# Kernel tuning notes

Measured on AMD Instinct MI355X. Metric: run time of the kernel, lower is better.

Reference implementation:

```python
import jax, jax.numpy as jnp
import numpy as np

KD_T = 4.0
PATCH_NUM = 64
MASK_NUM = 8
BATCH = 256
DIM = 2048
P = PATCH_NUM - MASK_NUM  # 56


def setup_inputs() -> dict:
    key = jax.random.key(0)
    k1, k2, k3 = jax.random.split(key, 3)
    ebg = jax.random.normal(k1, (BATCH, DIM), dtype=jnp.float32)
    ebp = jax.random.normal(k2, (P * BATCH, DIM), dtype=jnp.float32)
    labels = jax.random.randint(k3, (BATCH,), 0, 10, dtype=jnp.int64)
    return {"ebg": ebg, "ebp": ebp, "labels": labels}


def _kl(y_s, y_t, T):
    # Faithful to KLDiv with dim=0 on vectors: softmax over the feature axis,
    # F.kl_div(..., reduction='batchmean') on a length-D vector divides by D.
    D = y_s.shape[-1]
    log_p_s = jax.nn.log_softmax(y_s / T, axis=-1)
    log_p_t = jax.nn.log_softmax(y_t / T, axis=-1)
    p_t = jnp.exp(log_p_t)
    return jnp.sum(p_t * (log_p_t - log_p_s), axis=-1) * (T * T / D)


def reference(ebg, ebp, labels):
    sg = jax.lax.stop_gradient
    ebp_r = ebp.reshape(P, BATCH, DIM)          # [P, B, D]
    ebp_bar = ebp_r.mean(axis=0)                # [B, D]

    # soft_dil_loss: sum over batch of symmetric KD with detached targets
    soft_dil = jnp.sum(_kl(ebg, sg(ebp_bar), KD_T)) + jnp.sum(_kl(ebp_bar, sg(ebg), KD_T))

    # soft_dcl_loss: per (batch, patch) pair on squared differences
    ebp_t = jnp.transpose(ebp_r, (1, 0, 2))     # [B, P, D]
    dg = (ebg[:, None, :] - ebp_t) ** 2         # [B, P, D]
    db = (ebp_bar[:, None, :] - ebp_t) ** 2     # [B, P, D]
    soft_dcl = (jnp.sum(_kl(dg, db, KD_T)) + jnp.sum(_kl(db, dg, KD_T))) / P

    return (soft_dil, soft_dcl)
```

## Files before the change

### kernel.cpp

```cpp
#include <hip/hip_runtime.h>
#include <math.h>

#define DIM    2048
#define BATCH  256
#define PN     56
#define CHUNK  128
#define NCHUNK 4
#define NQ     4
#define QCOLS  (CHUNK * NCHUNK)
#define NBLK   (BATCH * NQ)
constexpr float KD_T = 4.0f;

__device__ __forceinline__ float wave_sum(float v) {
#pragma unroll
    for (int o = 32; o > 0; o >>= 1) v += __shfl_xor(v, o, 64);
    return v;
}
__device__ __forceinline__ float half_sum(float v) {
#pragma unroll
    for (int o = 16; o > 0; o >>= 1) v += __shfl_xor(v, o, 64);
    return v;
}
__device__ __forceinline__ double wave_sum_d(double v) {
#pragma unroll
    for (int o = 32; o > 0; o >>= 1) v += __shfl_xor(v, o, 64);
    return v;
}

__global__ void __launch_bounds__(256) fused_kernel(const float* __restrict__ ebg,
                                                    const float* __restrict__ ebp,
                                                    float* __restrict__ pdcl,
                                                    float* __restrict__ pdil,
                                                    double* __restrict__ dcl_acc,
                                                    unsigned* __restrict__ ticket)
{
    __shared__ float  ebp_s[PN * CHUNK];
    __shared__ float4 redbar[4][32];
    __shared__ float  bar_s[CHUNK];
    __shared__ float  redl[4][4];

    const int t    = threadIdx.x;
    const int lane = t & 63;
    const int wv   = t >> 6;
    const int sub  = lane >> 5;
    const int c32  = lane & 31;
    const int bid  = blockIdx.x;
    const int b    = bid >> 2;
    const int q    = bid & (NQ - 1);
    const float invT = 1.0f / KD_T;

    if (bid == 0 && t == 0) { *dcl_acc = 0.0; *ticket = 0u; }

    const size_t rowoff = (size_t)b * DIM + (size_t)q * QCOLS;

    float acc[7][4];
#pragma unroll
    for (int j = 0; j < 7; ++j)
#pragma unroll
        for (int k = 0; k < 4; ++k) acc[j][k] = 0.f;

    float dss = 0.f, dts = 0.f, dt1 = 0.f, dt2 = 0.f;

    for (int c = 0; c < NCHUNK; ++c) {
        const size_t cb = rowoff + (size_t)c * CHUNK;

        const int prow0 = t >> 5;
        const int cc4   = (t & 31) * 4;
        float4 vals[7];
#pragma unroll
        for (int it = 0; it < 7; ++it) {
            const int p = it * 8 + prow0;
            vals[it] = *(const float4*)(ebp + (size_t)p * (BATCH * DIM) + cb + cc4);
        }
        float4 bp = {0.f, 0.f, 0.f, 0.f};
#pragma unroll
        for (int it = 0; it < 7; ++it) {
            const int p = it * 8 + prow0;
            *(float4*)(ebp_s + p * CHUNK + cc4) = vals[it];
            bp.x += vals[it].x; bp.y += vals[it].y;
            bp.z += vals[it].z; bp.w += vals[it].w;
        }
        bp.x += __shfl_xor(bp.x, 32, 64);
        bp.y += __shfl_xor(bp.y, 32, 64);
        bp.z += __shfl_xor(bp.z, 32, 64);
        bp.w += __shfl_xor(bp.w, 32, 64);
        if (lane < 32) redbar[wv][lane] = bp;
        __syncthreads();
        if (t < 32) {
            float4 s0 = redbar[0][t], s1 = redbar[1][t],
                   s2 = redbar[2][t], s3 = redbar[3][t];
            float4 s;
            s.x = (s0.x + s1.x + s2.x + s3.x) * (1.0f / PN);
            s.y = (s0.y + s1.y + s2.y + s3.y) * (1.0f / PN);
            s.z = (s0.z + s1.z + s2.z + s3.z) * (1.0f / PN);
            s.w = (s0.w + s1.w + s2.w + s3.w) * (1.0f / PN);
            *(float4*)(bar_s + t * 4) = s;
        }
        __syncthreads();

        if (t < CHUNK) {
            float g = ebg[cb + t];
            float m = bar_s[t];
            float s = g * invT, tv = m * invT;
            float es = __expf(s), et = __expf(tv);
            float dd = tv - s;
            dss += es; dts += et;
            dt1 = fmaf(es, dd, dt1);
            dt2 = fmaf(et, dd, dt2);
        }

        const float4 g4 = *(const float4*)(ebg + cb + c32 * 4);
        const float4 m4 = *(const float4*)(bar_s + c32 * 4);
        const float gs[4] = {g4.x, g4.y, g4.z, g4.w};
        const float ms[4] = {m4.x, m4.y, m4.z, m4.w};
#pragma unroll
        for (int j = 0; j < 7; ++j) {
            const int row = wv * 14 + 2 * j + sub;
            float4 e = *(const float4*)(ebp_s + row * CHUNK + c32 * 4);
            float es_[4] = {e.x, e.y, e.z, e.w};
#pragma unroll
            for (int k = 0; k < 4; ++k) {
                float dg = gs[k] - es_[k];
                float db = ms[k] - es_[k];
                float a  = dg * dg * invT;
                float cc = db * db * invT;
                float ea = __expf(a), ec = __expf(cc);
                float d  = cc - a;
                acc[j][0] += ea;
                acc[j][1] += ec;
                acc[j][2] = fmaf(ea, d, acc[j][2]);
                acc[j][3] = fmaf(ec, d, acc[j][3]);
            }
        }
        __syncthreads();
    }

#pragma unroll
    for (int j = 0; j < 7; ++j) {
        float a0 = half_sum(acc[j][0]);
        float a1 = half_sum(acc[j][1]);
        float a2 = half_sum(acc[j][2]);
        float a3 = half_sum(acc[j][3]);
        if (c32 == 0) {
            const int row = wv * 14 + 2 * j + sub;
            float* qp = pdcl + (((size_t)row * BATCH + b) * NQ + q) * 4;
            qp[0] = a0; qp[1] = a1; qp[2] = a2; qp[3] = a3;
        }
    }
    dss = wave_sum(dss); dts = wave_sum(dts);
    dt1 = wave_sum(dt1); dt2 = wave_sum(dt2);
    if (lane == 0) { redl[wv][0] = dss; redl[wv][1] = dts; redl[wv][2] = dt1; redl[wv][3] = dt2; }
    __syncthreads();
    if (t == 0) {
        float* qp = pdil + (size_t)bid * 4;
#pragma unroll
        for (int k = 0; k < 4; ++k)
            qp[k] = redl[0][k] + redl[1][k] + redl[2][k] + redl[3][k];
    }
}

__global__ void __launch_bounds__(256) finalize_kernel(const float* __restrict__ pdcl,
                                                       const float* __restrict__ pdil,
                                                       double* __restrict__ dcl_acc,
                                                       unsigned* __restrict__ ticket,
                                                       float* __restrict__ out)
{
    __shared__ double sd[4];
    __shared__ int win_s;
    const int p = blockIdx.x, t = threadIdx.x, lane = t & 63, wv = t >> 6;

    const float* base = pdcl + ((size_t)p * BATCH + t) * NQ * 4;
    double A = 0.0, C = 0.0, T1 = 0.0, T2 = 0.0;
#pragma unroll
    for (int qq = 0; qq < NQ; ++qq) {
        float4 v = *(const float4*)(base + qq * 4);
        A += v.x; C += v.y; T1 += v.z; T2 += v.w;
    }
    double r = T2 / C - T1 / A;
    r = wave_sum_d(r);
    if (lane == 0) sd[wv] = r;
    __syncthreads();
    if (t == 0) {
        atomicAdd(dcl_acc, sd[0] + sd[1] + sd[2] + sd[3]);
        __threadfence();
        unsigned old = atomicAdd(ticket, 1u);
        win_s = (old == PN - 1) ? 1 : 0;
    }
    __syncthreads();
    if (!win_s) return;

    __threadfence();
    const float* dbase = pdil + (size_t)t * NQ * 4;
    double ss = 0.0, ts = 0.0, u1 = 0.0, u2 = 0.0;
#pragma unroll
    for (int qq = 0; qq < NQ; ++qq) {
        float4 v = *(const float4*)(dbase + qq * 4);
        ss += v.x; ts += v.y; u1 += v.z; u2 += v.w;
    }
    double vl = u2 / ts - u1 / ss;
    vl = wave_sum_d(vl);
    if (lane == 0) sd[wv] = vl;
    __syncthreads();
    if (t == 0) {
        double dcl = atomicAdd(dcl_acc, 0.0);
        const double kT2 = (double)KD_T * KD_T;
        out[0] = (float)((sd[0] + sd[1] + sd[2] + sd[3]) * (kT2 / DIM));
        out[1] = (float)(dcl * (kT2 / DIM / PN));
    }
}

extern "C" void kernel_launch(void* const* d_in, const int* in_sizes, int n_in,
                              void* d_out, int out_size, void* d_ws, size_t ws_size,
                              hipStream_t stream) {
    const float* ebg = (const float*)d_in[0];
    const float* ebp = (const float*)d_in[1];

    float*    pdcl    = (float*)d_ws;
    float*    pdil    = pdcl + (size_t)PN * BATCH * NQ * 4;
    double*   dcl_acc = (double*)(pdil + (size_t)NBLK * 4);
    unsigned* ticket  = (unsigned*)(dcl_acc + 1);

    fused_kernel<<<NBLK, 256, 0, stream>>>(ebg, ebp, pdcl, pdil, dcl_acc, ticket);
    finalize_kernel<<<PN, 256, 0, stream>>>(pdcl, pdil, dcl_acc, ticket, (float*)d_out);
}
```

Measured before the change: 183.4 us.

## Prefetch next chunk of ebp into registers and drop bar_s shared-memory stage

```diff
diff --git a/kernel.cpp b/kernel.cpp
--- a/kernel.cpp
+++ b/kernel.cpp
@@ -27,16 +27,15 @@
     return v;
 }
 
-__global__ void __launch_bounds__(256) fused_kernel(const float* __restrict__ ebg,
-                                                    const float* __restrict__ ebp,
-                                                    float* __restrict__ pdcl,
-                                                    float* __restrict__ pdil,
-                                                    double* __restrict__ dcl_acc,
-                                                    unsigned* __restrict__ ticket)
+__global__ void __launch_bounds__(256, 4) fused_kernel(const float* __restrict__ ebg,
+                                                       const float* __restrict__ ebp,
+                                                       float* __restrict__ pdcl,
+                                                       float* __restrict__ pdil,
+                                                       double* __restrict__ dcl_acc,
+                                                       unsigned* __restrict__ ticket)
 {
     __shared__ float  ebp_s[PN * CHUNK];
     __shared__ float4 redbar[4][32];
-    __shared__ float  bar_s[CHUNK];
     __shared__ float  redl[4][4];
 
     const int t    = threadIdx.x;
@@ -53,6 +52,11 @@
 
     const size_t rowoff = (size_t)b * DIM + (size_t)q * QCOLS;
 
+    float4 g_all[NCHUNK];
+#pragma unroll
+    for (int c = 0; c < NCHUNK; ++c)
+        g_all[c] = *(const float4*)(ebg + rowoff + c * CHUNK + c32 * 4);
+
     float acc[7][4];
 #pragma unroll
     for (int j = 0; j < 7; ++j)
@@ -61,17 +65,25 @@
 
     float dss = 0.f, dts = 0.f, dt1 = 0.f, dt2 = 0.f;
 
+    const int prow0 = t >> 5;
+    const int cc4   = (t & 31) * 4;
+    const float* pbase = ebp + (size_t)prow0 * (BATCH * DIM) + rowoff + cc4;
+
+    float4 vals[7];
+#pragma unroll
+    for (int it = 0; it < 7; ++it)
+        vals[it] = *(const float4*)(pbase + (size_t)(it * 8) * (BATCH * DIM));
+
+#pragma unroll
     for (int c = 0; c < NCHUNK; ++c) {
-        const size_t cb = rowoff + (size_t)c * CHUNK;
-
-        const int prow0 = t >> 5;
-        const int cc4   = (t & 31) * 4;
-        float4 vals[7];
-#pragma unroll
-        for (int it = 0; it < 7; ++it) {
-            const int p = it * 8 + prow0;
-            vals[it] = *(const float4*)(ebp + (size_t)p * (BATCH * DIM) + cb + cc4);
-        }
+        float4 vnext[7];
+        if (c + 1 < NCHUNK) {
+#pragma unroll
+            for (int it = 0; it < 7; ++it)
+                vnext[it] = *(const float4*)(pbase + (size_t)(it * 8) * (BATCH * DIM)
+                                             + (c + 1) * CHUNK);
+        }
+
         float4 bp = {0.f, 0.f, 0.f, 0.f};
 #pragma unroll
         for (int it = 0; it < 7; ++it) {
@@ -84,35 +96,32 @@
         bp.y += __shfl_xor(bp.y, 32, 64);
         bp.z += __shfl_xor(bp.z, 32, 64);
         bp.w += __shfl_xor(bp.w, 32, 64);
-        if (lane < 32) redbar[wv][lane] = bp;
+        if (sub == 0) redbar[wv][c32] = bp;
         __syncthreads();
-        if (t < 32) {
-            float4 s0 = redbar[0][t], s1 = redbar[1][t],
-                   s2 = redbar[2][t], s3 = redbar[3][t];
-            float4 s;
-            s.x = (s0.x + s1.x + s2.x + s3.x) * (1.0f / PN);
-            s.y = (s0.y + s1.y + s2.y + s3.y) * (1.0f / PN);
-            s.z = (s0.z + s1.z + s2.z + s3.z) * (1.0f / PN);
-            s.w = (s0.w + s1.w + s2.w + s3.w) * (1.0f / PN);
-            *(float4*)(bar_s + t * 4) = s;
-        }
-        __syncthreads();
-
-        if (t < CHUNK) {
-            float g = ebg[cb + t];
-            float m = bar_s[t];
-            float s = g * invT, tv = m * invT;
-            float es = __expf(s), et = __expf(tv);
-            float dd = tv - s;
-            dss += es; dts += et;
-            dt1 = fmaf(es, dd, dt1);
-            dt2 = fmaf(et, dd, dt2);
-        }
-
-        const float4 g4 = *(const float4*)(ebg + cb + c32 * 4);
-        const float4 m4 = *(const float4*)(bar_s + c32 * 4);
-        const float gs[4] = {g4.x, g4.y, g4.z, g4.w};
-        const float ms[4] = {m4.x, m4.y, m4.z, m4.w};
+
+        const float4 r0 = redbar[0][c32], r1 = redbar[1][c32],
+                     r2 = redbar[2][c32], r3 = redbar[3][c32];
+        float4 bar4;
+        bar4.x = (r0.x + r1.x + r2.x + r3.x) * (1.0f / PN);
+        bar4.y = (r0.y + r1.y + r2.y + r3.y) * (1.0f / PN);
+        bar4.z = (r0.z + r1.z + r2.z + r3.z) * (1.0f / PN);
+        bar4.w = (r0.w + r1.w + r2.w + r3.w) * (1.0f / PN);
+
+        const float gs[4] = {g_all[c].x, g_all[c].y, g_all[c].z, g_all[c].w};
+        const float ms[4] = {bar4.x, bar4.y, bar4.z, bar4.w};
+
+        if (wv == 0 && sub == 0) {
+#pragma unroll
+            for (int k = 0; k < 4; ++k) {
+                float s = gs[k] * invT, tv = ms[k] * invT;
+                float es = __expf(s), et = __expf(tv);
+                float dd = tv - s;
+                dss += es; dts += et;
+                dt1 = fmaf(es, dd, dt1);
+                dt2 = fmaf(et, dd, dt2);
+            }
+        }
+
 #pragma unroll
         for (int j = 0; j < 7; ++j) {
             const int row = wv * 14 + 2 * j + sub;
@@ -133,6 +142,11 @@
             }
         }
         __syncthreads();
+
+        if (c + 1 < NCHUNK) {
+#pragma unroll
+            for (int it = 0; it < 7; ++it) vals[it] = vnext[it];
+        }
     }
 
 #pragma unroll
```

Result: slower. 253.1 us (+38.0%).
